# Optimization experiments

Hardware: AMD Instinct MI355X
Metric: run time of the kernel (lower is better)

The kernel has to match this reference:

```python
import math
import jax, jax.numpy as jnp
import numpy as np

HEAD = 16
DIM = 1024
DH = DIM // HEAD
NEG = -100000000.0


def setup_inputs() -> dict:
    key = jax.random.key(0)
    ks = jax.random.split(key, 12)
    B, S, D = 2, 2048, DIM
    s = 1.0 / math.sqrt(D)
    return {
        "key": jax.random.normal(ks[0], (B, S, D), jnp.float32),
        "value": jax.random.normal(ks[1], (B, S, D), jnp.float32),
        "query": jax.random.normal(ks[2], (B, S, D), jnp.float32),
        "mask": jax.random.randint(ks[3], (B, 1, S, S), 0, 2) == 1,
        "Wq": jax.random.normal(ks[4], (D, D), jnp.float32) * s,
        "bq": jnp.zeros((D,), jnp.float32),
        "Wk": jax.random.normal(ks[5], (D, D), jnp.float32) * s,
        "bk": jnp.zeros((D,), jnp.float32),
        "Wv": jax.random.normal(ks[6], (D, D), jnp.float32) * s,
        "bv": jnp.zeros((D,), jnp.float32),
        "Wo": jax.random.normal(ks[7], (D, D), jnp.float32) * s,
        "bo": jnp.zeros((D,), jnp.float32),
    }


def _split_heads(x, b):
    # [B, S, D] -> [B, H, S, Dh]
    return x.reshape(b, -1, HEAD, DH).transpose(0, 2, 1, 3)


def reference(key, value, query, mask, Wq, bq, Wk, bk, Wv, bv, Wo, bo):
    b, k_len, d = key.shape
    q_len = query.shape[1]
    k_up = _split_heads(key @ Wk.T + bk, b)
    v_up = _split_heads(value @ Wv.T + bv, b)
    q_up = _split_heads(query @ Wq.T + bq, b) / math.sqrt(DH)
    scores = jnp.einsum("bhqd,bhkd->bhqk", q_up, k_up)
    scores = jnp.where(mask, NEG, scores)
    attn = jax.nn.softmax(scores, axis=-1)
    # dropout is identity in eval/reference mode
    context = jnp.einsum("bhqk,bhkd->bhqd", attn, v_up)
    context = context.transpose(0, 2, 1, 3).reshape(b, q_len, d)
    out = context @ Wo.T + bo
    return out, attn
```

## Files before the change

### kernel.cpp

```cpp
#include <hip/hip_runtime.h>
#include <stdint.h>

#define S_LEN 2048
#define D_MODEL 1024
#define N_HEAD 16
#define D_HEAD 64
#define N_BATCH 2
#define M_TOK (N_BATCH * S_LEN)

typedef unsigned short u16;
typedef unsigned int u32;
typedef __attribute__((ext_vector_type(8))) short bf16x8;
typedef __attribute__((ext_vector_type(4))) short s16x4;
typedef __attribute__((ext_vector_type(4))) float f32x4;
typedef __attribute__((ext_vector_type(4))) unsigned short u16x4;

#define MFMA16(a, b, c) __builtin_amdgcn_mfma_f32_16x16x32_bf16((a), (b), (c), 0, 0, 0)

#if defined(__has_builtin)
#if __has_builtin(__builtin_amdgcn_mfma_f32_16x16x16bf16_1k)
#define HAVE_MFMA_16x16x16 1
#define MFMA_PV(a, b, c) __builtin_amdgcn_mfma_f32_16x16x16bf16_1k((a), (b), (c), 0, 0, 0)
#endif
#endif

__device__ __forceinline__ u16 f2bf(float f) {
  unsigned int u = __float_as_uint(f);
  u = (u + 0x7FFFu + ((u >> 16) & 1u)) >> 16;
  return (u16)u;
}

__device__ __forceinline__ void gload_lds16(const u16* g, u16* l) {
  __builtin_amdgcn_global_load_lds((const __attribute__((address_space(1))) void*)g,
                                   (__attribute__((address_space(3))) void*)l, 16, 0, 0);
}

#define N4BIG (M_TOK * D_MODEL / 4)
#define N4W (D_MODEL * D_MODEL / 4)
__global__ __launch_bounds__(256) void cvt7_kernel(
    const float* __restrict__ sk, const float* __restrict__ sv, const float* __restrict__ sq,
    const float* __restrict__ swq, const float* __restrict__ swk, const float* __restrict__ swv,
    const float* __restrict__ swo, u16* __restrict__ dk, u16* __restrict__ dv, u16* __restrict__ dq,
    u16* __restrict__ dwq, u16* __restrict__ dwk, u16* __restrict__ dwv, u16* __restrict__ dwo) {
  const float* s;
  u16* d;
  int n4;
  switch (blockIdx.y) {
    case 0: s = sk; d = dk; n4 = N4BIG; break;
    case 1: s = sv; d = dv; n4 = N4BIG; break;
    case 2: s = sq; d = dq; n4 = N4BIG; break;
    case 3: s = swq; d = dwq; n4 = N4W; break;
    case 4: s = swk; d = dwk; n4 = N4W; break;
    case 5: s = swv; d = dwv; n4 = N4W; break;
    default: s = swo; d = dwo; n4 = N4W; break;
  }
  int i = blockIdx.x * blockDim.x + threadIdx.x;
  int stride = gridDim.x * blockDim.x;
  for (; i < n4; i += stride) {
    float4 v = ((const float4*)s)[i];
    u16x4 o = {f2bf(v.x), f2bf(v.y), f2bf(v.z), f2bf(v.w)};
    ((u16x4*)d)[i] = o;
  }
}

__global__ __launch_bounds__(256) void pack_mask(const int* __restrict__ mask,
                                                 unsigned long long* __restrict__ packed) {
  int wid = (blockIdx.x * blockDim.x + threadIdx.x) >> 6;
  int lane = threadIdx.x & 63;
  int nw = (gridDim.x * blockDim.x) >> 6;
  const int NW64 = M_TOK * (S_LEN / 64);
  for (int widx = wid; widx < NW64; widx += nw) {
    int m = mask[(size_t)widx * 64 + lane];
    unsigned long long bits = __ballot(m != 0);
    if (lane == 0) packed[widx] = bits;
  }
}

__device__ __forceinline__ void gemm_body(const u16* __restrict__ A, const u16* __restrict__ Bw,
                                          const float* __restrict__ bias, void* __restrict__ Cout,
                                          float scale, int outmode) {
  __shared__ u16 As[128 * 32];
  __shared__ u16 Bs[128 * 32];
  const int K = D_MODEL, N = D_MODEL;
  int tid = threadIdx.x;
  int w = tid >> 6, lane = tid & 63, lg = lane >> 4, lr = lane & 15;
  int m0 = blockIdx.x * 128, n0 = blockIdx.y * 128;
  int wr = w >> 1, wc = w & 1;
  f32x4 acc[4][4] = {};
  int r0 = tid >> 2;
  int r1 = 64 + (tid >> 2);
  int kk0 = (tid & 3) * 8;
  for (int kb = 0; kb < K; kb += 32) {
    gload_lds16(A + (size_t)(m0 + r0) * K + kb + kk0, As + w * 512);
    gload_lds16(A + (size_t)(m0 + r1) * K + kb + kk0, As + 2048 + w * 512);
    gload_lds16(Bw + (size_t)(n0 + r0) * K + kb + kk0, Bs + w * 512);
    gload_lds16(Bw + (size_t)(n0 + r1) * K + kb + kk0, Bs + 2048 + w * 512);
    __syncthreads();
    bf16x8 af[4], bfr[4];
#pragma unroll
    for (int i = 0; i < 4; i++)
      af[i] = *(const bf16x8*)(As + (wr * 64 + i * 16 + lr) * 32 + lg * 8);
#pragma unroll
    for (int i = 0; i < 4; i++)
      bfr[i] = *(const bf16x8*)(Bs + (wc * 64 + i * 16 + lr) * 32 + lg * 8);
#pragma unroll
    for (int mi = 0; mi < 4; mi++)
#pragma unroll
      for (int ni = 0; ni < 4; ni++)
        acc[mi][ni] = MFMA16(af[mi], bfr[ni], acc[mi][ni]);
    __syncthreads();
  }
#pragma unroll
  for (int mi = 0; mi < 4; mi++)
#pragma unroll
    for (int ni = 0; ni < 4; ni++) {
      int col = n0 + wc * 64 + ni * 16 + lr;
      float bv = bias[col];
      if (outmode == 2) {
        int row0 = m0 + wr * 64 + mi * 16 + lg * 4;
        int bb = row0 >> 11, ss = row0 & (S_LEN - 1);
        u16x4 pk;
#pragma unroll
        for (int r = 0; r < 4; r++) pk[r] = f2bf((acc[mi][ni][r] + bv) * scale);
        *(u16x4*)((u16*)Cout + ((size_t)((bb * N_HEAD + (col >> 6)) * D_HEAD + (col & 63)) * S_LEN + ss)) = pk;
      } else {
#pragma unroll
        for (int r = 0; r < 4; r++) {
          int row = m0 + wr * 64 + mi * 16 + lg * 4 + r;
          float v = (acc[mi][ni][r] + bv) * scale;
          if (outmode == 1)
            ((float*)Cout)[(size_t)row * N + col] = v;
          else
            ((u16*)Cout)[(size_t)row * N + col] = f2bf(v);
        }
      }
    }
}

#define QSCALE 0.18033688011112042f

__global__ __launch_bounds__(256) void proj3_kernel(
    const u16* __restrict__ kbf, const u16* __restrict__ vbf, const u16* __restrict__ qbf,
    const u16* __restrict__ wkb, const u16* __restrict__ wvb, const u16* __restrict__ wqb,
    const float* __restrict__ bk, const float* __restrict__ bv, const float* __restrict__ bq,
    u16* __restrict__ kup, u16* __restrict__ vtg, u16* __restrict__ qup) {
  int z = blockIdx.z;
  if (z == 0)
    gemm_body(kbf, wkb, bk, kup, 1.0f, 0);
  else if (z == 1)
    gemm_body(vbf, wvb, bv, vtg, 1.0f, 2);
  else
    gemm_body(qbf, wqb, bq, qup, QSCALE, 0);
}

__global__ __launch_bounds__(256) void gemm_out_kernel(const u16* __restrict__ A,
                                                       const u16* __restrict__ Bw,
                                                       const float* __restrict__ bias,
                                                       float* __restrict__ C) {
  gemm_body(A, Bw, bias, C, 1.0f, 1);
}

__global__ __launch_bounds__(512, 4) void attn_kernel(
    const u16* __restrict__ Qup, const u16* __restrict__ Kup, const u16* __restrict__ Vt,
    const u32* __restrict__ mpack, float* __restrict__ attn_out, u16* __restrict__ ctx) {
  __shared__ u16 kbuf[2][64 * 64];
  __shared__ u16 vbuf[2][64 * 64];
#if !defined(HAVE_MFMA_16x16x16)
  __shared__ u16 pbuf[8][16 * 64];
#endif
  int tid = threadIdx.x;
  int w = tid >> 6, lane = tid & 63, lg = lane >> 4, lr = lane & 15;

  int fb = blockIdx.x;
  int logical = (fb & 7) * 64 + (fb >> 3);
  int qx = logical & 15;
  int h = (logical >> 4) & 15;
  int b = logical >> 8;
  int q0 = qx * 128;
  int q = q0 + w * 16 + lr;
  const float NEGV = -100000000.0f;

  bf16x8 qf0, qf1;
  {
    const u16* qrow = Qup + (size_t)(b * S_LEN + q) * D_MODEL + h * D_HEAD;
    qf0 = *(const bf16x8*)(qrow + lg * 8);
    qf1 = *(const bf16x8*)(qrow + 32 + lg * 8);
  }
  const u16* Kb = Kup + (size_t)(b * S_LEN) * D_MODEL + h * D_HEAD;
  const u16* Vb = Vt + (size_t)(b * N_HEAD + h) * D_HEAD * S_LEN;
  const u32* mrow = mpack + (size_t)(b * S_LEN + q) * (S_LEN / 32);
  float* attn_b = attn_out + ((size_t)(b * N_HEAD + h) * S_LEN + q) * S_LEN;

  int srow = tid >> 3;
  int scs = (tid & 7) ^ (srow & 7);
  const u16* KgBase = Kb + (size_t)srow * D_MODEL + scs * 8;
  const u16* VgBase = Vb + (size_t)srow * S_LEN + scs * 8;
  const int sw = lr & 7;

  float lsum = 0.f;
  gload_lds16(KgBase, &kbuf[0][w * 512]);
  __syncthreads();
  for (int kt = 0; kt < 32; kt++) {
    int cur = kt & 1;
    if (kt < 31) gload_lds16(KgBase + (size_t)(kt + 1) * 64 * D_MODEL, &kbuf[cur ^ 1][w * 512]);
    const u16* kc = &kbuf[cur][0];
    uint2 mm = *(const uint2*)(mrow + kt * 2);
#pragma unroll
    for (int t = 0; t < 4; t++) {
      int rK = t * 16 + lr;
      bf16x8 k0 = *(const bf16x8*)(kc + rK * 64 + ((lg ^ sw) << 3));
      bf16x8 k1 = *(const bf16x8*)(kc + rK * 64 + (((lg + 4) ^ sw) << 3));
      f32x4 a = {0.f, 0.f, 0.f, 0.f};
      a = MFMA16(k0, qf0, a);
      a = MFMA16(k1, qf1, a);
      u32 wbits = (t < 2) ? mm.x : mm.y;
#pragma unroll
      for (int r = 0; r < 4; r++) {
        int j = (t * 16 + lg * 4 + r) & 31;
        float s = ((wbits >> j) & 1u) ? NEGV : a[r];
        lsum += exp2f(s);
      }
    }
    __syncthreads();
  }
  lsum += __shfl_xor(lsum, 16);
  lsum += __shfl_xor(lsum, 32);
  float inv_l = lsum > 0.f ? 1.0f / lsum : 0.f;

  f32x4 ctxacc[4] = {};
  gload_lds16(KgBase, &kbuf[0][w * 512]);
  gload_lds16(VgBase, &vbuf[0][w * 512]);
  __syncthreads();
  for (int kt = 0; kt < 32; kt++) {
    int cur = kt & 1;
    if (kt < 31) {
      gload_lds16(KgBase + (size_t)(kt + 1) * 64 * D_MODEL, &kbuf[cur ^ 1][w * 512]);
      gload_lds16(VgBase + (size_t)(kt + 1) * 64, &vbuf[cur ^ 1][w * 512]);
    }
    const u16* kc = &kbuf[cur][0];
    const u16* vc = &vbuf[cur][0];
    uint2 mm = *(const uint2*)(mrow + kt * 2);
    int kb = kt * 64;
#if defined(HAVE_MFMA_16x16x16)
    s16x4 apv[4];
#endif
#pragma unroll
    for (int t = 0; t < 4; t++) {
      int rK = t * 16 + lr;
      bf16x8 k0 = *(const bf16x8*)(kc + rK * 64 + ((lg ^ sw) << 3));
      bf16x8 k1 = *(const bf16x8*)(kc + rK * 64 + (((lg + 4) ^ sw) << 3));
      f32x4 a = {0.f, 0.f, 0.f, 0.f};
      a = MFMA16(k0, qf0, a);
      a = MFMA16(k1, qf1, a);
      u32 wbits = (t < 2) ? mm.x : mm.y;
      f32x4 p;
      u16x4 pb;
#pragma unroll
      for (int r = 0; r < 4; r++) {
        int j = (t * 16 + lg * 4 + r) & 31;
        float s = ((wbits >> j) & 1u) ? NEGV : a[r];
        float pv = exp2f(s) * inv_l;
        p[r] = pv;
        pb[r] = f2bf(pv);
      }
      *(f32x4*)(attn_b + kb + t * 16 + lg * 4) = p;
#if defined(HAVE_MFMA_16x16x16)
      s16x4 ap = {(short)pb[0], (short)pb[1], (short)pb[2], (short)pb[3]};
      apv[t] = ap;
#else
      *(u16x4*)(&pbuf[w][lr * 64 + ((((t * 2) + (lg >> 1)) ^ sw) << 3) + ((lg & 1) << 2)]) = pb;
#endif
    }
#if defined(HAVE_MFMA_16x16x16)
#pragma unroll
    for (int t = 0; t < 4; t++) {
#pragma unroll
      for (int d = 0; d < 4; d++) {
        s16x4 vf = *(const s16x4*)(vc + (d * 16 + lr) * 64 +
                                   ((((t * 2) + (lg >> 1)) ^ sw) << 3) + ((lg & 1) << 2));
        ctxacc[d] = MFMA_PV(apv[t], vf, ctxacc[d]);
      }
    }
#else
    u16* pw = &pbuf[w][0];
    bf16x8 pa0 = *(const bf16x8*)(pw + lr * 64 + ((lg ^ sw) << 3));
    bf16x8 pa1 = *(const bf16x8*)(pw + lr * 64 + (((lg + 4) ^ sw) << 3));
#pragma unroll
    for (int t = 0; t < 4; t++) {
      int rV = t * 16 + lr;
      bf16x8 v0 = *(const bf16x8*)(vc + rV * 64 + ((lg ^ sw) << 3));
      bf16x8 v1 = *(const bf16x8*)(vc + rV * 64 + (((lg + 4) ^ sw) << 3));
      ctxacc[t] = MFMA16(pa0, v0, ctxacc[t]);
      ctxacc[t] = MFMA16(pa1, v1, ctxacc[t]);
    }
#endif
    __syncthreads();
  }

#pragma unroll
  for (int t = 0; t < 4; t++)
#pragma unroll
    for (int r = 0; r < 4; r++) {
      int sq = q0 + w * 16 + lg * 4 + r;
      ctx[(size_t)(b * S_LEN + sq) * D_MODEL + h * D_HEAD + t * 16 + lr] = f2bf(ctxacc[t][r]);
    }
}

#define O_KBF 0u
#define O_VBF 4194304u
#define O_QBF 8388608u
#define O_WQ 12582912u
#define O_WK 13631488u
#define O_WV 14680064u
#define O_WO 15728640u
#define O_QUP 16777216u
#define O_KUP 20971520u
#define O_VUP 25165824u
#define O_CTX 29360128u

extern "C" void kernel_launch(void* const* d_in, const int* in_sizes, int n_in,
                              void* d_out, int out_size, void* d_ws, size_t ws_size,
                              hipStream_t stream) {
  const float* key = (const float*)d_in[0];
  const float* value = (const float*)d_in[1];
  const float* query = (const float*)d_in[2];
  const int* mask = (const int*)d_in[3];
  const float* Wq = (const float*)d_in[4];
  const float* bq = (const float*)d_in[5];
  const float* Wk = (const float*)d_in[6];
  const float* bk = (const float*)d_in[7];
  const float* Wv = (const float*)d_in[8];
  const float* bv = (const float*)d_in[9];
  const float* Wo = (const float*)d_in[10];
  const float* bo = (const float*)d_in[11];

  u16* ws = (u16*)d_ws;
  u16* kbf = ws + O_KBF;
  u16* vbf = ws + O_VBF;
  u16* qbf = ws + O_QBF;
  u16* wqb = ws + O_WQ;
  u16* wkb = ws + O_WK;
  u16* wvb = ws + O_WV;
  u16* wob = ws + O_WO;
  u16* qup = ws + O_QUP;
  u16* kup = ws + O_KUP;
  u16* vtg = ws + O_VUP;
  u16* ctxb = ws + O_CTX;

  float* out = (float*)d_out;
  float* attn = out + (size_t)N_BATCH * S_LEN * D_MODEL;

  cvt7_kernel<<<dim3(512, 7), 256, 0, stream>>>(key, value, query, Wq, Wk, Wv, Wo, kbf, vbf, qbf,
                                                wqb, wkb, wvb, wob);
  proj3_kernel<<<dim3(32, 8, 3), 256, 0, stream>>>(kbf, vbf, qbf, wkb, wvb, wqb, bk, bv, bq, kup,
                                                   vtg, qup);
  pack_mask<<<1024, 256, 0, stream>>>(mask, (unsigned long long*)kbf);
  attn_kernel<<<512, 512, 0, stream>>>(qup, kup, vtg, (const u32*)kbf, attn, ctxb);
  gemm_out_kernel<<<dim3(32, 8), 256, 0, stream>>>(ctxb, wob, bo, out);
}
```

Before: 354.8 us.

## Double key tile to 128 and replace syncthreads with explicit vmcnt waits

After: 338.7 us. 4.5% less time.

```diff
diff --git a/kernel.cpp b/kernel.cpp
--- a/kernel.cpp
+++ b/kernel.cpp
@@ -23,6 +23,8 @@
 #define MFMA_PV(a, b, c) __builtin_amdgcn_mfma_f32_16x16x16bf16_1k((a), (b), (c), 0, 0, 0)
 #endif
 #endif
+
+#define WAITCNT(n) asm volatile("s_waitcnt vmcnt(" #n ")" ::: "memory")
 
 __device__ __forceinline__ u16 f2bf(float f) {
   unsigned int u = __float_as_uint(f);
@@ -163,8 +165,8 @@
 __global__ __launch_bounds__(512, 4) void attn_kernel(
     const u16* __restrict__ Qup, const u16* __restrict__ Kup, const u16* __restrict__ Vt,
     const u32* __restrict__ mpack, float* __restrict__ attn_out, u16* __restrict__ ctx) {
-  __shared__ u16 kbuf[2][64 * 64];
-  __shared__ u16 vbuf[2][64 * 64];
+  __shared__ u16 kbuf[2][128 * 64];
+  __shared__ u16 vbuf[2][64 * 128];
 #if !defined(HAVE_MFMA_16x16x16)
   __shared__ u16 pbuf[8][16 * 64];
 #endif
@@ -191,119 +193,151 @@
   const u32* mrow = mpack + (size_t)(b * S_LEN + q) * (S_LEN / 32);
   float* attn_b = attn_out + ((size_t)(b * N_HEAD + h) * S_LEN + q) * S_LEN;
 
-  int srow = tid >> 3;
-  int scs = (tid & 7) ^ (srow & 7);
-  const u16* KgBase = Kb + (size_t)srow * D_MODEL + scs * 8;
-  const u16* VgBase = Vb + (size_t)srow * S_LEN + scs * 8;
+  int krow = tid >> 3;
+  int kchunk = (tid & 7) ^ (krow & 7);
+  const u16* KgA = Kb + (size_t)krow * D_MODEL + kchunk * 8;
+  int vrow = tid >> 4;
+  int vchunk = ((tid & 15) ^ (vrow & 7));
+  const u16* VgA = Vb + (size_t)vrow * S_LEN + vchunk * 8;
   const int sw = lr & 7;
 
-  float lsum = 0.f;
-  gload_lds16(KgBase, &kbuf[0][w * 512]);
-  __syncthreads();
-  for (int kt = 0; kt < 32; kt++) {
+#define STAGE_K(bn, ktn)                                                    \
+  do {                                                                      \
+    const u16* _s = KgA + (size_t)(ktn) * 128 * D_MODEL;                    \
+    gload_lds16(_s, &kbuf[bn][0] + w * 512);                                \
+    gload_lds16(_s + (size_t)64 * D_MODEL, &kbuf[bn][4096] + w * 512);      \
+  } while (0)
+#define STAGE_V(bn, ktn)                                                    \
+  do {                                                                      \
+    const u16* _s = VgA + (size_t)(ktn) * 128;                              \
+    gload_lds16(_s, &vbuf[bn][0] + w * 512);                                \
+    gload_lds16(_s + (size_t)32 * S_LEN, &vbuf[bn][4096] + w * 512);        \
+  } while (0)
+
+  float lsA = 0.f, lsB = 0.f;
+  STAGE_K(0, 0);
+  for (int kt = 0; kt < 16; kt++) {
     int cur = kt & 1;
-    if (kt < 31) gload_lds16(KgBase + (size_t)(kt + 1) * 64 * D_MODEL, &kbuf[cur ^ 1][w * 512]);
+    if (kt < 15) STAGE_K(cur ^ 1, kt + 1);
+    uint4 mm = *(const uint4*)(mrow + kt * 4);
+    if (kt < 15) {
+      WAITCNT(3);
+    } else {
+      WAITCNT(1);
+    }
+    __builtin_amdgcn_s_barrier();
+    __builtin_amdgcn_sched_barrier(0);
     const u16* kc = &kbuf[cur][0];
-    uint2 mm = *(const uint2*)(mrow + kt * 2);
-#pragma unroll
-    for (int t = 0; t < 4; t++) {
-      int rK = t * 16 + lr;
-      bf16x8 k0 = *(const bf16x8*)(kc + rK * 64 + ((lg ^ sw) << 3));
-      bf16x8 k1 = *(const bf16x8*)(kc + rK * 64 + (((lg + 4) ^ sw) << 3));
+#pragma unroll
+    for (int t = 0; t < 8; t++) {
+      const u16* kr = kc + (t * 16 + lr) * 64;
+      bf16x8 k0 = *(const bf16x8*)(kr + ((lg ^ sw) << 3));
+      bf16x8 k1 = *(const bf16x8*)(kr + (((lg + 4) ^ sw) << 3));
       f32x4 a = {0.f, 0.f, 0.f, 0.f};
       a = MFMA16(k0, qf0, a);
       a = MFMA16(k1, qf1, a);
-      u32 wbits = (t < 2) ? mm.x : mm.y;
+      u32 wbits = (t >> 1) == 0 ? mm.x : (t >> 1) == 1 ? mm.y : (t >> 1) == 2 ? mm.z : mm.w;
 #pragma unroll
       for (int r = 0; r < 4; r++) {
         int j = (t * 16 + lg * 4 + r) & 31;
         float s = ((wbits >> j) & 1u) ? NEGV : a[r];
-        lsum += exp2f(s);
+        if (r & 1)
+          lsB += exp2f(s);
+        else
+          lsA += exp2f(s);
       }
     }
-    __syncthreads();
-  }
+    __builtin_amdgcn_sched_barrier(0);
+    __builtin_amdgcn_s_barrier();
+  }
+  float lsum = lsA + lsB;
   lsum += __shfl_xor(lsum, 16);
   lsum += __shfl_xor(lsum, 32);
   float inv_l = lsum > 0.f ? 1.0f / lsum : 0.f;
 
   f32x4 ctxacc[4] = {};
-  gload_lds16(KgBase, &kbuf[0][w * 512]);
-  gload_lds16(VgBase, &vbuf[0][w * 512]);
-  __syncthreads();
-  for (int kt = 0; kt < 32; kt++) {
+  STAGE_K(0, 0);
+  STAGE_V(0, 0);
+  for (int kt = 0; kt < 16; kt++) {
     int cur = kt & 1;
-    if (kt < 31) {
-      gload_lds16(KgBase + (size_t)(kt + 1) * 64 * D_MODEL, &kbuf[cur ^ 1][w * 512]);
-      gload_lds16(VgBase + (size_t)(kt + 1) * 64, &vbuf[cur ^ 1][w * 512]);
-    }
+    if (kt < 15) {
+      STAGE_K(cur ^ 1, kt + 1);
+      STAGE_V(cur ^ 1, kt + 1);
+    }
+    uint4 mm = *(const uint4*)(mrow + kt * 4);
+    if (kt < 15) {
+      WAITCNT(5);
+    } else {
+      WAITCNT(1);
+    }
+    __builtin_amdgcn_s_barrier();
+    __builtin_amdgcn_sched_barrier(0);
     const u16* kc = &kbuf[cur][0];
     const u16* vc = &vbuf[cur][0];
-    uint2 mm = *(const uint2*)(mrow + kt * 2);
-    int kb = kt * 64;
+#pragma unroll
+    for (int h2 = 0; h2 < 2; h2++) {
+#pragma unroll
+      for (int tt = 0; tt < 4; tt++) {
+        const int t = h2 * 4 + tt;
+        const u16* kr = kc + (t * 16 + lr) * 64;
+        bf16x8 k0 = *(const bf16x8*)(kr + ((lg ^ sw) << 3));
+        bf16x8 k1 = *(const bf16x8*)(kr + (((lg + 4) ^ sw) << 3));
+        f32x4 a = {0.f, 0.f, 0.f, 0.f};
+        a = MFMA16(k0, qf0, a);
+        a = MFMA16(k1, qf1, a);
+        u32 wbits = (t >> 1) == 0 ? mm.x : (t >> 1) == 1 ? mm.y : (t >> 1) == 2 ? mm.z : mm.w;
+        f32x4 p;
+        u16x4 pb;
+#pragma unroll
+        for (int r = 0; r < 4; r++) {
+          int j = (t * 16 + lg * 4 + r) & 31;
+          float s = ((wbits >> j) & 1u) ? NEGV : a[r];
+          float pv = exp2f(s) * inv_l;
+          p[r] = pv;
+          pb[r] = f2bf(pv);
+        }
+        *(f32x4*)(attn_b + kt * 128 + t * 16 + lg * 4) = p;
 #if defined(HAVE_MFMA_16x16x16)
-    s16x4 apv[4];
-#endif
-#pragma unroll
-    for (int t = 0; t < 4; t++) {
-      int rK = t * 16 + lr;
-      bf16x8 k0 = *(const bf16x8*)(kc + rK * 64 + ((lg ^ sw) << 3));
-      bf16x8 k1 = *(const bf16x8*)(kc + rK * 64 + (((lg + 4) ^ sw) << 3));
-      f32x4 a = {0.f, 0.f, 0.f, 0.f};
-      a = MFMA16(k0, qf0, a);
-      a = MFMA16(k1, qf1, a);
-      u32 wbits = (t < 2) ? mm.x : mm.y;
-      f32x4 p;
-      u16x4 pb;
-#pragma unroll
-      for (int r = 0; r < 4; r++) {
-        int j = (t * 16 + lg * 4 + r) & 31;
-        float s = ((wbits >> j) & 1u) ? NEGV : a[r];
-        float pv = exp2f(s) * inv_l;
-        p[r] = pv;
-        pb[r] = f2bf(pv);
+        s16x4 ap = {(short)pb[0], (short)pb[1], (short)pb[2], (short)pb[3]};
+#pragma unroll
+        for (int d = 0; d < 4; d++) {
+          s16x4 vf = *(const s16x4*)(vc + (d * 16 + lr) * 128 +
+                                     (((t * 2 + (lg >> 1)) ^ sw) << 3) + ((lg & 1) << 2));
+          ctxacc[d] = MFMA_PV(ap, vf, ctxacc[d]);
+        }
+#else
+        *(u16x4*)(&pbuf[w][lr * 64 + ((((tt * 2) + (lg >> 1)) ^ sw) << 3) + ((lg & 1) << 2)]) = pb;
+#endif
       }
-      *(f32x4*)(attn_b + kb + t * 16 + lg * 4) = p;
-#if defined(HAVE_MFMA_16x16x16)
-      s16x4 ap = {(short)pb[0], (short)pb[1], (short)pb[2], (short)pb[3]};
-      apv[t] = ap;
-#else
-      *(u16x4*)(&pbuf[w][lr * 64 + ((((t * 2) + (lg >> 1)) ^ sw) << 3) + ((lg & 1) << 2)]) = pb;
-#endif
-    }
-#if defined(HAVE_MFMA_16x16x16)
-#pragma unroll
-    for (int t = 0; t < 4; t++) {
-#pragma unroll
-      for (int d = 0; d < 4; d++) {
-        s16x4 vf = *(const s16x4*)(vc + (d * 16 + lr) * 64 +
-                                   ((((t * 2) + (lg >> 1)) ^ sw) << 3) + ((lg & 1) << 2));
-        ctxacc[d] = MFMA_PV(apv[t], vf, ctxacc[d]);
+#if !defined(HAVE_MFMA_16x16x16)
+      {
+        u16* pw = &pbuf[w][0];
+        bf16x8 pa0 = *(const bf16x8*)(pw + lr * 64 + ((lg ^ sw) << 3));
+        bf16x8 pa1 = *(const bf16x8*)(pw + lr * 64 + (((lg + 4) ^ sw) << 3));
+#pragma unroll
+        for (int d = 0; d < 4; d++) {
+          const u16* vr = vc + (d * 16 + lr) * 128 + (h2 << 6);
+          bf16x8 v0 = *(const bf16x8*)(vr + ((lg ^ sw) << 3));
+          bf16x8 v1 = *(const bf16x8*)(vr + (((lg + 4) ^ sw) << 3));
+          ctxacc[d] = MFMA16(pa0, v0, ctxacc[d]);
+          ctxacc[d] = MFMA16(pa1, v1, ctxacc[d]);
+        }
       }
-    }
-#else
-    u16* pw = &pbuf[w][0];
-    bf16x8 pa0 = *(const bf16x8*)(pw + lr * 64 + ((lg ^ sw) << 3));
-    bf16x8 pa1 = *(const bf16x8*)(pw + lr * 64 + (((lg + 4) ^ sw) << 3));
-#pragma unroll
-    for (int t = 0; t < 4; t++) {
-      int rV = t * 16 + lr;
-      bf16x8 v0 = *(const bf16x8*)(vc + rV * 64 + ((lg ^ sw) << 3));
-      bf16x8 v1 = *(const bf16x8*)(vc + rV * 64 + (((lg + 4) ^ sw) << 3));
-      ctxacc[t] = MFMA16(pa0, v0, ctxacc[t]);
-      ctxacc[t] = MFMA16(pa1, v1, ctxacc[t]);
-    }
-#endif
-    __syncthreads();
-  }
-
-#pragma unroll
-  for (int t = 0; t < 4; t++)
+#endif
+    }
+    __builtin_amdgcn_sched_barrier(0);
+    if (kt < 15) __builtin_amdgcn_s_barrier();
+  }
+
+#pragma unroll
+  for (int d = 0; d < 4; d++)
 #pragma unroll
     for (int r = 0; r < 4; r++) {
       int sq = q0 + w * 16 + lg * 4 + r;
-      ctx[(size_t)(b * S_LEN + sq) * D_MODEL + h * D_HEAD + t * 16 + lr] = f2bf(ctxacc[t][r]);
-    }
+      ctx[(size_t)(b * S_LEN + sq) * D_MODEL + h * D_HEAD + d * 16 + lr] = f2bf(ctxacc[d][r]);
+    }
+#undef STAGE_K
+#undef STAGE_V
 }
 
 #define O_KBF 0u
```

## Deepen attention K/V LDS pipeline to four buffers with explicit vmcnt waits

Applied to the files above, without the earlier changes.

Result: slower. 362.8 us (+2.3%).

```diff
diff --git a/kernel.cpp b/kernel.cpp
--- a/kernel.cpp
+++ b/kernel.cpp
@@ -23,6 +23,8 @@
 #define MFMA_PV(a, b, c) __builtin_amdgcn_mfma_f32_16x16x16bf16_1k((a), (b), (c), 0, 0, 0)
 #endif
 #endif
+
+#define WAITCNT(n) asm volatile("s_waitcnt vmcnt(" #n ")" ::: "memory")
 
 __device__ __forceinline__ u16 f2bf(float f) {
   unsigned int u = __float_as_uint(f);
@@ -163,8 +165,8 @@
 __global__ __launch_bounds__(512, 4) void attn_kernel(
     const u16* __restrict__ Qup, const u16* __restrict__ Kup, const u16* __restrict__ Vt,
     const u32* __restrict__ mpack, float* __restrict__ attn_out, u16* __restrict__ ctx) {
-  __shared__ u16 kbuf[2][64 * 64];
-  __shared__ u16 vbuf[2][64 * 64];
+  __shared__ u16 kbuf[4][64 * 64];
+  __shared__ u16 vbuf[4][64 * 64];
 #if !defined(HAVE_MFMA_16x16x16)
   __shared__ u16 pbuf[8][16 * 64];
 #endif
@@ -192,118 +194,228 @@
   float* attn_b = attn_out + ((size_t)(b * N_HEAD + h) * S_LEN + q) * S_LEN;
 
   int srow = tid >> 3;
-  int scs = (tid & 7) ^ (srow & 7);
-  const u16* KgBase = Kb + (size_t)srow * D_MODEL + scs * 8;
-  const u16* VgBase = Vb + (size_t)srow * S_LEN + scs * 8;
+  int schunk = (tid & 7) ^ (srow & 7);
+  const u16* KgA = Kb + (size_t)srow * D_MODEL + schunk * 8;
+  const u16* VgA = Vb + (size_t)srow * S_LEN + schunk * 8;
   const int sw = lr & 7;
 
-  float lsum = 0.f;
-  gload_lds16(KgBase, &kbuf[0][w * 512]);
-  __syncthreads();
-  for (int kt = 0; kt < 32; kt++) {
-    int cur = kt & 1;
-    if (kt < 31) gload_lds16(KgBase + (size_t)(kt + 1) * 64 * D_MODEL, &kbuf[cur ^ 1][w * 512]);
-    const u16* kc = &kbuf[cur][0];
-    uint2 mm = *(const uint2*)(mrow + kt * 2);
-#pragma unroll
-    for (int t = 0; t < 4; t++) {
-      int rK = t * 16 + lr;
-      bf16x8 k0 = *(const bf16x8*)(kc + rK * 64 + ((lg ^ sw) << 3));
-      bf16x8 k1 = *(const bf16x8*)(kc + rK * 64 + (((lg + 4) ^ sw) << 3));
-      f32x4 a = {0.f, 0.f, 0.f, 0.f};
-      a = MFMA16(k0, qf0, a);
-      a = MFMA16(k1, qf1, a);
-      u32 wbits = (t < 2) ? mm.x : mm.y;
-#pragma unroll
-      for (int r = 0; r < 4; r++) {
-        int j = (t * 16 + lg * 4 + r) & 31;
-        float s = ((wbits >> j) & 1u) ? NEGV : a[r];
-        lsum += exp2f(s);
-      }
-    }
-    __syncthreads();
-  }
+#define STAGE_K(bn, ktn) gload_lds16(KgA + (size_t)(ktn) * 64 * D_MODEL, &kbuf[bn][w * 512])
+#define STAGE_V(bn, ktn) gload_lds16(VgA + (size_t)(ktn) * 64, &vbuf[bn][w * 512])
+#define BARRIER()                      \
+  __builtin_amdgcn_s_barrier();        \
+  __builtin_amdgcn_sched_barrier(0)
+#define SEAL() __builtin_amdgcn_sched_barrier(0)
+
+  float lsA = 0.f, lsB = 0.f;
+
+#define P0_BODY(KT, MMU)                                                   \
+  {                                                                        \
+    const u16* kc = &kbuf[(KT) & 3][0];                                    \
+    _Pragma("unroll") for (int t = 0; t < 4; t++) {                        \
+      const u16* kr = kc + (t * 16 + lr) * 64;                             \
+      bf16x8 k0 = *(const bf16x8*)(kr + ((lg ^ sw) << 3));                 \
+      bf16x8 k1 = *(const bf16x8*)(kr + (((lg + 4) ^ sw) << 3));           \
+      f32x4 a = {0.f, 0.f, 0.f, 0.f};                                      \
+      a = MFMA16(k0, qf0, a);                                              \
+      a = MFMA16(k1, qf1, a);                                              \
+      u32 wbits = (t < 2) ? (MMU).x : (MMU).y;                             \
+      _Pragma("unroll") for (int r = 0; r < 4; r++) {                      \
+        int j = (t * 16 + lg * 4 + r) & 31;                                \
+        float s = ((wbits >> j) & 1u) ? NEGV : a[r];                       \
+        if (r & 1) lsB += exp2f(s); else lsA += exp2f(s);                  \
+      }                                                                    \
+    }                                                                      \
+  }
+
+#define P0_FULL(KT, MMU, MML, WN)                          \
+  do {                                                     \
+    MML = *(const uint2*)(mrow + ((KT) + 1) * 2);          \
+    STAGE_K(((KT) + 2) & 3, (KT) + 2);                     \
+    WAITCNT(WN);                                           \
+    BARRIER();                                             \
+    P0_BODY(KT, MMU);                                      \
+    SEAL();                                                \
+  } while (0)
+#define P0_NOST(KT, MMU, MML, WN)                          \
+  do {                                                     \
+    MML = *(const uint2*)(mrow + ((KT) + 1) * 2);          \
+    WAITCNT(WN);                                           \
+    BARRIER();                                             \
+    P0_BODY(KT, MMU);                                      \
+    SEAL();                                                \
+  } while (0)
+#define P0_LAST(KT, MMU, WN)                               \
+  do {                                                     \
+    WAITCNT(WN);                                           \
+    BARRIER();                                             \
+    P0_BODY(KT, MMU);                                      \
+    SEAL();                                                \
+  } while (0)
+
+  uint2 mA, mB;
+  mA = *(const uint2*)(mrow);
+  STAGE_K(0, 0);
+  STAGE_K(1, 1);
+  P0_FULL(0, mA, mB, 3);
+  P0_FULL(1, mB, mA, 3);
+  P0_FULL(2, mA, mB, 3);
+  P0_FULL(3, mB, mA, 3);
+  for (int m = 1; m < 7; m++) {
+    const int b4 = m * 4;
+    P0_FULL(b4 + 0, mA, mB, 3);
+    P0_FULL(b4 + 1, mB, mA, 3);
+    P0_FULL(b4 + 2, mA, mB, 3);
+    P0_FULL(b4 + 3, mB, mA, 3);
+  }
+  P0_FULL(28, mA, mB, 3);
+  P0_FULL(29, mB, mA, 3);
+  P0_NOST(30, mA, mB, 2);
+  P0_LAST(31, mB, 0);
+
+  float lsum = lsA + lsB;
   lsum += __shfl_xor(lsum, 16);
   lsum += __shfl_xor(lsum, 32);
   float inv_l = lsum > 0.f ? 1.0f / lsum : 0.f;
 
   f32x4 ctxacc[4] = {};
-  gload_lds16(KgBase, &kbuf[0][w * 512]);
-  gload_lds16(VgBase, &vbuf[0][w * 512]);
-  __syncthreads();
-  for (int kt = 0; kt < 32; kt++) {
-    int cur = kt & 1;
-    if (kt < 31) {
-      gload_lds16(KgBase + (size_t)(kt + 1) * 64 * D_MODEL, &kbuf[cur ^ 1][w * 512]);
-      gload_lds16(VgBase + (size_t)(kt + 1) * 64, &vbuf[cur ^ 1][w * 512]);
-    }
-    const u16* kc = &kbuf[cur][0];
-    const u16* vc = &vbuf[cur][0];
-    uint2 mm = *(const uint2*)(mrow + kt * 2);
-    int kb = kt * 64;
+
 #if defined(HAVE_MFMA_16x16x16)
-    s16x4 apv[4];
+#define P1_BODY(KT, MMU)                                                   \
+  {                                                                        \
+    const u16* kc = &kbuf[(KT) & 3][0];                                    \
+    const u16* vc = &vbuf[(KT) & 3][0];                                    \
+    _Pragma("unroll") for (int t = 0; t < 4; t++) {                        \
+      const u16* kr = kc + (t * 16 + lr) * 64;                             \
+      bf16x8 k0 = *(const bf16x8*)(kr + ((lg ^ sw) << 3));                 \
+      bf16x8 k1 = *(const bf16x8*)(kr + (((lg + 4) ^ sw) << 3));           \
+      f32x4 a = {0.f, 0.f, 0.f, 0.f};                                      \
+      a = MFMA16(k0, qf0, a);                                              \
+      a = MFMA16(k1, qf1, a);                                              \
+      u32 wbits = (t < 2) ? (MMU).x : (MMU).y;                             \
+      f32x4 p;                                                             \
+      u16x4 pb;                                                            \
+      _Pragma("unroll") for (int r = 0; r < 4; r++) {                      \
+        int j = (t * 16 + lg * 4 + r) & 31;                                \
+        float s = ((wbits >> j) & 1u) ? NEGV : a[r];                       \
+        float pv = exp2f(s) * inv_l;                                       \
+        p[r] = pv;                                                         \
+        pb[r] = f2bf(pv);                                                  \
+      }                                                                    \
+      *(f32x4*)(attn_b + (KT) * 64 + t * 16 + lg * 4) = p;                 \
+      s16x4 ap = {(short)pb[0], (short)pb[1], (short)pb[2], (short)pb[3]}; \
+      _Pragma("unroll") for (int d = 0; d < 4; d++) {                      \
+        s16x4 vf = *(const s16x4*)(vc + (d * 16 + lr) * 64 +               \
+                                   (((t * 2 + (lg >> 1)) ^ sw) << 3) +     \
+                                   ((lg & 1) << 2));                       \
+        ctxacc[d] = MFMA_PV(ap, vf, ctxacc[d]);                            \
+      }                                                                    \
+    }                                                                      \
+  }
+#else
+#define P1_BODY(KT, MMU)                                                   \
+  {                                                                        \
+    const u16* kc = &kbuf[(KT) & 3][0];                                    \
+    const u16* vc = &vbuf[(KT) & 3][0];                                    \
+    u16* pw = &pbuf[w][0];                                                 \
+    _Pragma("unroll") for (int t = 0; t < 4; t++) {                        \
+      const u16* kr = kc + (t * 16 + lr) * 64;                             \
+      bf16x8 k0 = *(const bf16x8*)(kr + ((lg ^ sw) << 3));                 \
+      bf16x8 k1 = *(const bf16x8*)(kr + (((lg + 4) ^ sw) << 3));           \
+      f32x4 a = {0.f, 0.f, 0.f, 0.f};                                      \
+      a = MFMA16(k0, qf0, a);                                              \
+      a = MFMA16(k1, qf1, a);                                              \
+      u32 wbits = (t < 2) ? (MMU).x : (MMU).y;                             \
+      f32x4 p;                                                             \
+      u16x4 pb;                                                            \
+      _Pragma("unroll") for (int r = 0; r < 4; r++) {                      \
+        int j = (t * 16 + lg * 4 + r) & 31;                                \
+        float s = ((wbits >> j) & 1u) ? NEGV : a[r];                       \
+        float pv = exp2f(s) * inv_l;                                       \
+        p[r] = pv;                                                         \
+        pb[r] = f2bf(pv);                                                  \
+      }                                                                    \
+      *(f32x4*)(attn_b + (KT) * 64 + t * 16 + lg * 4) = p;                 \
+      *(u16x4*)(pw + lr * 64 + (((t * 2 + (lg >> 1)) ^ sw) << 3) +         \
+                ((lg & 1) << 2)) = pb;                                     \
+    }                                                                      \
+    bf16x8 pa0 = *(const bf16x8*)(pw + lr * 64 + ((lg ^ sw) << 3));        \
+    bf16x8 pa1 = *(const bf16x8*)(pw + lr * 64 + (((lg + 4) ^ sw) << 3));  \
+    _Pragma("unroll") for (int d = 0; d < 4; d++) {                        \
+      const u16* vr = vc + (d * 16 + lr) * 64;                             \
+      bf16x8 v0 = *(const bf16x8*)(vr + ((lg ^ sw) << 3));                 \
+      bf16x8 v1 = *(const bf16x8*)(vr + (((lg + 4) ^ sw) << 3));           \
+      ctxacc[d] = MFMA16(pa0, v0, ctxacc[d]);                              \
+      ctxacc[d] = MFMA16(pa1, v1, ctxacc[d]);                              \
+    }                                                                      \
+  }
 #endif
-#pragma unroll
-    for (int t = 0; t < 4; t++) {
-      int rK = t * 16 + lr;
-      bf16x8 k0 = *(const bf16x8*)(kc + rK * 64 + ((lg ^ sw) << 3));
-      bf16x8 k1 = *(const bf16x8*)(kc + rK * 64 + (((lg + 4) ^ sw) << 3));
-      f32x4 a = {0.f, 0.f, 0.f, 0.f};
-      a = MFMA16(k0, qf0, a);
-      a = MFMA16(k1, qf1, a);
-      u32 wbits = (t < 2) ? mm.x : mm.y;
-      f32x4 p;
-      u16x4 pb;
-#pragma unroll
-      for (int r = 0; r < 4; r++) {
-        int j = (t * 16 + lg * 4 + r) & 31;
-        float s = ((wbits >> j) & 1u) ? NEGV : a[r];
-        float pv = exp2f(s) * inv_l;
-        p[r] = pv;
-        pb[r] = f2bf(pv);
-      }
-      *(f32x4*)(attn_b + kb + t * 16 + lg * 4) = p;
-#if defined(HAVE_MFMA_16x16x16)
-      s16x4 ap = {(short)pb[0], (short)pb[1], (short)pb[2], (short)pb[3]};
-      apv[t] = ap;
-#else
-      *(u16x4*)(&pbuf[w][lr * 64 + ((((t * 2) + (lg >> 1)) ^ sw) << 3) + ((lg & 1) << 2)]) = pb;
-#endif
-    }
-#if defined(HAVE_MFMA_16x16x16)
-#pragma unroll
-    for (int t = 0; t < 4; t++) {
-#pragma unroll
-      for (int d = 0; d < 4; d++) {
-        s16x4 vf = *(const s16x4*)(vc + (d * 16 + lr) * 64 +
-                                   ((((t * 2) + (lg >> 1)) ^ sw) << 3) + ((lg & 1) << 2));
-        ctxacc[d] = MFMA_PV(apv[t], vf, ctxacc[d]);
-      }
-    }
-#else
-    u16* pw = &pbuf[w][0];
-    bf16x8 pa0 = *(const bf16x8*)(pw + lr * 64 + ((lg ^ sw) << 3));
-    bf16x8 pa1 = *(const bf16x8*)(pw + lr * 64 + (((lg + 4) ^ sw) << 3));
-#pragma unroll
-    for (int t = 0; t < 4; t++) {
-      int rV = t * 16 + lr;
-      bf16x8 v0 = *(const bf16x8*)(vc + rV * 64 + ((lg ^ sw) << 3));
-      bf16x8 v1 = *(const bf16x8*)(vc + rV * 64 + (((lg + 4) ^ sw) << 3));
-      ctxacc[t] = MFMA16(pa0, v0, ctxacc[t]);
-      ctxacc[t] = MFMA16(pa1, v1, ctxacc[t]);
-    }
-#endif
-    __syncthreads();
-  }
-
-#pragma unroll
-  for (int t = 0; t < 4; t++)
+
+#define P1_FULL(KT, MMU, MML, WN)                          \
+  do {                                                     \
+    MML = *(const uint2*)(mrow + ((KT) + 1) * 2);          \
+    STAGE_K(((KT) + 2) & 3, (KT) + 2);                     \
+    STAGE_V(((KT) + 2) & 3, (KT) + 2);                     \
+    WAITCNT(WN);                                           \
+    BARRIER();                                             \
+    P1_BODY(KT, MMU);                                      \
+    SEAL();                                                \
+  } while (0)
+#define P1_NOST(KT, MMU, MML, WN)                          \
+  do {                                                     \
+    MML = *(const uint2*)(mrow + ((KT) + 1) * 2);          \
+    WAITCNT(WN);                                           \
+    BARRIER();                                             \
+    P1_BODY(KT, MMU);                                      \
+    SEAL();                                                \
+  } while (0)
+#define P1_LAST(KT, MMU, WN)                               \
+  do {                                                     \
+    WAITCNT(WN);                                           \
+    BARRIER();                                             \
+    P1_BODY(KT, MMU);                                      \
+    SEAL();                                                \
+  } while (0)
+
+  mA = *(const uint2*)(mrow);
+  STAGE_K(0, 0);
+  STAGE_V(0, 0);
+  STAGE_K(1, 1);
+  STAGE_V(1, 1);
+  P1_FULL(0, mA, mB, 5);
+  P1_FULL(1, mB, mA, 9);
+  P1_FULL(2, mA, mB, 9);
+  P1_FULL(3, mB, mA, 9);
+  for (int m = 1; m < 7; m++) {
+    const int b4 = m * 4;
+    P1_FULL(b4 + 0, mA, mB, 9);
+    P1_FULL(b4 + 1, mB, mA, 9);
+    P1_FULL(b4 + 2, mA, mB, 9);
+    P1_FULL(b4 + 3, mB, mA, 9);
+  }
+  P1_FULL(28, mA, mB, 9);
+  P1_FULL(29, mB, mA, 9);
+  P1_NOST(30, mA, mB, 7);
+  P1_LAST(31, mB, 4);
+
+#pragma unroll
+  for (int d = 0; d < 4; d++)
 #pragma unroll
     for (int r = 0; r < 4; r++) {
       int sq = q0 + w * 16 + lg * 4 + r;
-      ctx[(size_t)(b * S_LEN + sq) * D_MODEL + h * D_HEAD + t * 16 + lr] = f2bf(ctxacc[t][r]);
+      ctx[(size_t)(b * S_LEN + sq) * D_MODEL + h * D_HEAD + d * 16 + lr] = f2bf(ctxacc[d][r]);
     }
+#undef STAGE_K
+#undef STAGE_V
+#undef BARRIER
+#undef SEAL
+#undef P0_BODY
+#undef P0_FULL
+#undef P0_NOST
+#undef P0_LAST
+#undef P1_BODY
+#undef P1_FULL
+#undef P1_NOST
+#undef P1_LAST
 }
 
 #define O_KBF 0u
```
